# Kernel optimization log

Measured on AMD Instinct MI355X. Metric: run time of the kernel, lower is better.

## Reference

```python
import jax, jax.numpy as jnp
import numpy as np

D_EMB, N_HEADS = 1024, 16
D_K = D_EMB // N_HEADS

def setup_inputs() -> dict:
    key = jax.random.key(0)
    ks = jax.random.split(key, 5)
    scale = 0.02
    return {
        "n": jax.random.normal(ks[0], (2, 2048, D_EMB), dtype=jnp.float32),
        "W_q": jax.random.normal(ks[1], (D_EMB, D_EMB), dtype=jnp.float32) * scale,
        "W_k": jax.random.normal(ks[2], (D_EMB, D_EMB), dtype=jnp.float32) * scale,
        "W_v": jax.random.normal(ks[3], (D_EMB, D_EMB), dtype=jnp.float32) * scale,
        "W_o": jax.random.normal(ks[4], (D_EMB, D_EMB), dtype=jnp.float32) * scale,
    }

def reference(n, W_q, W_k, W_v, W_o):
    B, S, _ = n.shape
    # torch Linear(bias=False): y = x @ W.T, W is [out, in]
    def proj(x, W):
        y = jnp.einsum('bsd,ed->bse', x, W)
        return y.reshape(B, S, N_HEADS, D_K).transpose(0, 2, 1, 3)  # [B,H,S,Dk]
    Q, K, V = proj(n, W_q), proj(n, W_k), proj(n, W_v)
    A = jnp.einsum('bhqd,bhkd->bhqk', Q, K) * (D_K ** -0.5)
    A = jnp.clip(A, -5.0, 5.0)
    A = jax.nn.softmax(A, axis=-1)
    ctx = jnp.einsum('bhqk,bhkd->bhqd', A, V)  # [B,H,S,Dk]
    ctx = ctx.transpose(0, 2, 1, 3).reshape(B, S, D_EMB)
    return jnp.einsum('bsd,ed->bse', ctx, W_o)
```

## Files before the change

kernel.cpp:

```cpp
#include <hip/hip_runtime.h>
#include <hip/hip_bf16.h>
#include <stdint.h>

typedef __attribute__((ext_vector_type(4))) float floatx4;
typedef __attribute__((ext_vector_type(8))) short shortx8;
typedef __attribute__((ext_vector_type(4))) unsigned short ushortx4;
typedef __attribute__((ext_vector_type(8))) unsigned short ushortx8;
typedef __attribute__((ext_vector_type(2))) uint32_t uintx2;

#define MFMA16(a, b, c) __builtin_amdgcn_mfma_f32_16x16x32_bf16((a), (b), (c), 0, 0, 0)

__device__ inline unsigned short f2bf(float f) {
    union { float f; uint32_t u; } v; v.f = f;
    uint32_t u = v.u;
    return (unsigned short)((u + 0x7FFFu + ((u >> 16) & 1u)) >> 16);
}

#if defined(__has_builtin) && __has_builtin(__builtin_amdgcn_cvt_pk_bf16_f32)
__device__ inline uint32_t pkbf(float a, float b) {
    auto r = __builtin_amdgcn_cvt_pk_bf16_f32(a, b);
    union { decltype(r) v; uint32_t u; } x; x.v = r; return x.u;
}
#else
__device__ inline uint32_t pkbf(float a, float b) {
    return ((uint32_t)f2bf(b) << 16) | f2bf(a);
}
#endif

#if defined(__has_builtin) && __has_builtin(__builtin_amdgcn_exp2f)
#define EXP2F(x) __builtin_amdgcn_exp2f(x)
#else
#define EXP2F(x) __expf((x) * 0.69314718056f)
#endif

#if defined(__has_builtin) && __has_builtin(__builtin_amdgcn_fmed3f)
#define CLAMP3(x, lo, hi) __builtin_amdgcn_fmed3f((x), (lo), (hi))
#else
#define CLAMP3(x, lo, hi) fminf(fmaxf((x), (lo)), (hi))
#endif

__device__ inline void gl2lds16(const void* g, void* l) {
    __builtin_amdgcn_global_load_lds(
        (const __attribute__((address_space(1))) void*)(uintptr_t)g,
        (__attribute__((address_space(3))) void*)(uintptr_t)l, 16, 0, 0);
}

__global__ void convert_all(const float* __restrict__ n, const float* __restrict__ wq,
                            const float* __restrict__ wk, const float* __restrict__ wv,
                            const float* __restrict__ wo,
                            unsigned short* __restrict__ nb, unsigned short* __restrict__ wqb,
                            unsigned short* __restrict__ wkb, unsigned short* __restrict__ wvb,
                            unsigned short* __restrict__ wob) {
    int i = blockIdx.x * 256 + threadIdx.x;
    const float* src; unsigned short* dst; int off;
    if (i < 1048576) { src = n; dst = nb; off = i; }
    else {
        int j = i - 1048576; int r = j >> 18; int o = j & 262143;
        src = (r == 0) ? wq : (r == 1) ? wk : (r == 2) ? wv : wo;
        dst = (r == 0) ? wqb : (r == 1) ? wkb : (r == 2) ? wvb : wob;
        off = o;
    }
    floatx4 f = ((const floatx4*)src)[off];
    uintx2 u;
    u.x = pkbf(f.x, f.y); u.y = pkbf(f.z, f.w);
    ((uintx2*)dst)[off] = u;
}

__device__ inline void gemm_tile_128(const unsigned short* __restrict__ A,
                                     const unsigned short* __restrict__ B,
                                     unsigned short* sA, unsigned short* sB,
                                     floatx4 acc[4][4]) {
    const int tid = threadIdx.x, w = tid >> 6, l = tid & 63;
    const int c = l & 15, quad = l >> 4;
    const int wm = (w >> 1) * 64, wn = (w & 1) * 64;
    for (int kt = 0; kt < 16; ++kt) {
        #pragma unroll
        for (int r = 0; r < 4; ++r) {
            int row = r * 32 + w * 8 + (l >> 3);
            int cb  = (l & 7) ^ (row & 7);
            gl2lds16(A + row * 1024 + kt * 64 + cb * 8, (char*)sA + r * 4096 + w * 1024 + l * 16);
            gl2lds16(B + row * 1024 + kt * 64 + cb * 8, (char*)sB + r * 4096 + w * 1024 + l * 16);
        }
        __syncthreads();
        #pragma unroll
        for (int ks = 0; ks < 2; ++ks) {
            shortx8 af[4], bfr[4];
            #pragma unroll
            for (int i2 = 0; i2 < 4; ++i2) {
                int ra = wm + i2 * 16 + c;
                af[i2] = *(const shortx8*)((const char*)sA + ra * 128 + (((ks * 4 + quad) ^ (ra & 7)) * 16));
                int rb = wn + i2 * 16 + c;
                bfr[i2] = *(const shortx8*)((const char*)sB + rb * 128 + (((ks * 4 + quad) ^ (rb & 7)) * 16));
            }
            #pragma unroll
            for (int i2 = 0; i2 < 4; ++i2)
                #pragma unroll
                for (int j2 = 0; j2 < 4; ++j2)
                    acc[i2][j2] = MFMA16(af[i2], bfr[j2], acc[i2][j2]);
        }
        __syncthreads();
    }
}

__global__ void gemm_qkv(const unsigned short* __restrict__ nb,
                         const unsigned short* __restrict__ wqb,
                         const unsigned short* __restrict__ wkb,
                         const unsigned short* __restrict__ wvb,
                         unsigned short* __restrict__ Qb, unsigned short* __restrict__ Kb,
                         unsigned short* __restrict__ VTg) {
    __shared__ unsigned short sAB[2 * 128 * 64];
    unsigned short* sA = sAB;
    unsigned short* sB = sAB + 128 * 64;
    const int mt = blockIdx.x, nt = blockIdx.y;
    const int region = nt >> 3, nl0 = (nt & 7) * 128;
    const unsigned short* W = (region == 0) ? wqb : (region == 1) ? wkb : wvb;
    floatx4 acc[4][4] = {};
    gemm_tile_128(nb + mt * 128 * 1024, W + nl0 * 1024, sA, sB, acc);
    const int tid = threadIdx.x, w = tid >> 6, l = tid & 63, c = l & 15, quad = l >> 4;
    const int wm = (w >> 1) * 64, wn = (w & 1) * 64;
    if (region < 2) {
        unsigned short* O = (region == 0) ? Qb : Kb;
        #pragma unroll
        for (int i2 = 0; i2 < 4; ++i2)
            #pragma unroll
            for (int j2 = 0; j2 < 4; ++j2)
                #pragma unroll
                for (int r = 0; r < 4; ++r) {
                    int row = wm + i2 * 16 + quad * 4 + r, col = wn + j2 * 16 + c;
                    sAB[row * 128 + col] = f2bf(acc[i2][j2][r]);
                }
        __syncthreads();
        #pragma unroll
        for (int t = 0; t < 8; ++t) {
            int off = t * 4096 + tid * 16;
            int row = off >> 8, colb = off & 255;
            *(ushortx8*)((char*)(O + (mt * 128 + row) * 1024 + nl0) + colb) =
                *(const ushortx8*)((const char*)sAB + off);
        }
    } else {
        const int hh = w & 1, tt = w >> 1;
        char* img = (char*)sAB + (hh * 2 + tt) * 8192;
        #pragma unroll
        for (int i2 = 0; i2 < 4; ++i2)
            #pragma unroll
            for (int j2 = 0; j2 < 4; ++j2) {
                int d = j2 * 16 + c;
                int blk = (i2 >> 1) * 4 + quad;
                int phys = blk ^ (d & 7);
                uintx2 v;
                v.x = pkbf(acc[i2][j2][0], acc[i2][j2][1]);
                v.y = pkbf(acc[i2][j2][2], acc[i2][j2][3]);
                *(uintx2*)(img + d * 128 + phys * 16 + (i2 & 1) * 8) = v;
            }
        __syncthreads();
        const int h0 = (nt & 7) * 2, t0 = mt * 2;
        #pragma unroll
        for (int g = 0; g < 8; ++g) {
            int off = g * 4096 + tid * 16;
            int hsel = off >> 14, within = off & 16383;
            *(ushortx8*)((char*)VTg + (h0 + hsel) * 524288 + t0 * 8192 + within) =
                *(const ushortx8*)((const char*)sAB + off);
        }
    }
}

__global__ void __launch_bounds__(256) gemm_out(const unsigned short* __restrict__ ctx,
                         const unsigned short* __restrict__ wob,
                         float* __restrict__ out) {
    __shared__ unsigned short sA[128 * 64];
    __shared__ unsigned short sB[64 * 64];
    __shared__ float sC[64 * 64];
    const int mt = blockIdx.x, nt = blockIdx.y;
    const unsigned short* A = ctx + mt * 128 * 1024;
    const unsigned short* B = wob + nt * 64 * 1024;
    const int tid = threadIdx.x, w = tid >> 6, l = tid & 63, c = l & 15, quad = l >> 4;
    const int srow = w * 8 + (l >> 3), scb = l & 7;
    floatx4 acc[2][4] = {};
    for (int kt = 0; kt < 16; ++kt) {
        #pragma unroll
        for (int r = 0; r < 4; ++r) {
            int row = r * 32 + srow, cb = scb ^ (row & 7);
            gl2lds16(A + row * 1024 + kt * 64 + cb * 8, (char*)sA + r * 4096 + w * 1024 + l * 16);
        }
        #pragma unroll
        for (int r = 0; r < 2; ++r) {
            int row = r * 32 + srow, cb = scb ^ (row & 7);
            gl2lds16(B + row * 1024 + kt * 64 + cb * 8, (char*)sB + r * 4096 + w * 1024 + l * 16);
        }
        __syncthreads();
        #pragma unroll
        for (int ks = 0; ks < 2; ++ks) {
            shortx8 af[2], bf2[4];
            #pragma unroll
            for (int i2 = 0; i2 < 2; ++i2) {
                int ra = w * 32 + i2 * 16 + c;
                af[i2] = *(const shortx8*)((const char*)sA + ra * 128 + (((ks * 4 + quad) ^ (ra & 7)) * 16));
            }
            #pragma unroll
            for (int j2 = 0; j2 < 4; ++j2) {
                int rb = j2 * 16 + c;
                bf2[j2] = *(const shortx8*)((const char*)sB + rb * 128 + (((ks * 4 + quad) ^ (rb & 7)) * 16));
            }
            #pragma unroll
            for (int i2 = 0; i2 < 2; ++i2)
                #pragma unroll
                for (int j2 = 0; j2 < 4; ++j2)
                    acc[i2][j2] = MFMA16(af[i2], bf2[j2], acc[i2][j2]);
        }
        __syncthreads();
    }
    #pragma unroll
    for (int half = 0; half < 2; ++half) {
        if ((w >> 1) == half) {
            #pragma unroll
            for (int i2 = 0; i2 < 2; ++i2)
                #pragma unroll
                for (int j2 = 0; j2 < 4; ++j2)
                    #pragma unroll
                    for (int r = 0; r < 4; ++r) {
                        int row = (w & 1) * 32 + i2 * 16 + quad * 4 + r, col = j2 * 16 + c;
                        sC[row * 64 + col] = acc[i2][j2][r];
                    }
        }
        __syncthreads();
        #pragma unroll
        for (int t = 0; t < 4; ++t) {
            int off = t * 4096 + tid * 16;
            int row = off >> 8, colb = off & 255;
            *(floatx4*)((char*)(out + (mt * 128 + half * 64 + row) * 1024 + nt * 64) + colb) =
                *(const floatx4*)((const char*)sC + off);
        }
        __syncthreads();
    }
}

__global__ void __launch_bounds__(256, 2) attn(const unsigned short* __restrict__ Qb,
                     const unsigned short* __restrict__ Kb,
                     const unsigned short* __restrict__ VTg, unsigned short* __restrict__ ctx) {
    __shared__ char lds[81920];
    const int qt = blockIdx.x, h = blockIdx.y, b = blockIdx.z;
    const int tid = threadIdx.x, w = tid >> 6, l = tid & 63, c = l & 15, quad = l >> 4;
    const int tok0 = b * 2048 + qt * 128;
    const int srow = w * 8 + (l >> 3);
    const int cb = (l & 7) ^ (srow & 7);
    #pragma unroll
    for (int r = 0; r < 4; ++r)
        gl2lds16(Qb + (tok0 + r * 32 + srow) * 1024 + h * 64 + cb * 8, lds + r * 4096 + w * 1024 + l * 16);
    const unsigned short* Kbase = Kb + b * 2048 * 1024 + h * 64;
    const char* Vbase = (const char*)VTg + h * 524288 + (size_t)b * 262144;
    const char* Ksrc = (const char*)(Kbase + srow * 1024 + cb * 8);
    #define STAGE_K(kt, t) { _Pragma("unroll") for (int r = 0; r < 2; ++r) \
        gl2lds16(Ksrc + (size_t)(kt) * 131072 + r * 65536, lds + 16384 + (t) * 8192 + r * 4096 + w * 1024 + l * 16); }
    #define STAGE_V(kt, t) { _Pragma("unroll") for (int r = 0; r < 2; ++r) \
        gl2lds16(Vbase + (kt) * 8192 + r * 4096 + w * 1024 + l * 16, lds + 49152 + (t) * 8192 + r * 4096 + w * 1024 + l * 16); }
    STAGE_K(0, 0) STAGE_V(0, 0) STAGE_K(1, 1) STAGE_V(1, 1)
    __syncthreads();
    int lb[2];
    lb[0] = c * 128 + ((quad ^ (c & 7)) * 16);
    lb[1] = c * 128 + (((4 + quad) ^ (c & 7)) * 16);
    shortx8 qf[2][2];
    #pragma unroll
    for (int ks = 0; ks < 2; ++ks)
        #pragma unroll
        for (int qb = 0; qb < 2; ++qb)
            qf[ks][qb] = *(const shortx8*)(lds + (w * 2 + qb) * 2048 + lb[ks]);
    floatx4 cacc[4][2] = {};
    float lacc[2] = {0.f, 0.f};
    const float SC = 0.18033688f;
    const float CLIP = 7.2134752f;

    #define COMPUTE_S(t, s) { _Pragma("unroll") for (int ks = 0; ks < 2; ++ks) { \
        shortx8 ak[4]; \
        _Pragma("unroll") for (int j = 0; j < 4; ++j) \
            ak[j] = *(const shortx8*)(lds + 16384 + (t) * 8192 + j * 2048 + lb[ks]); \
        _Pragma("unroll") for (int j = 0; j < 4; ++j) \
            _Pragma("unroll") for (int qb = 0; qb < 2; ++qb) \
                s[qb][j] = MFMA16(ak[j], qf[ks][qb], s[qb][j]); } }

    #define SOFTMAX_T(s) { _Pragma("unroll") for (int qb = 0; qb < 2; ++qb) { \
        float rs = 0.f; \
        _Pragma("unroll") for (int j = 0; j < 4; ++j) \
            _Pragma("unroll") for (int r = 0; r < 4; ++r) { \
                float v = EXP2F(CLAMP3(s[qb][j][r] * SC, -CLIP, CLIP)); \
                s[qb][j][r] = v; rs += v; } \
        rs += __shfl_xor(rs, 16); rs += __shfl_xor(rs, 32); \
        lacc[qb] += rs; } }

    #define PV_T(t, s) { _Pragma("unroll") for (int chunk = 0; chunk < 2; ++chunk) { \
        shortx8 av[4]; \
        _Pragma("unroll") for (int di = 0; di < 4; ++di) \
            av[di] = *(const shortx8*)(lds + 49152 + (t) * 8192 + di * 2048 + lb[chunk]); \
        shortx8 p[2]; \
        _Pragma("unroll") for (int qb = 0; qb < 2; ++qb) { \
            union { shortx8 v; uint32_t u[4]; } pk; \
            pk.u[0] = pkbf(s[qb][2 * chunk][0], s[qb][2 * chunk][1]); \
            pk.u[1] = pkbf(s[qb][2 * chunk][2], s[qb][2 * chunk][3]); \
            pk.u[2] = pkbf(s[qb][2 * chunk + 1][0], s[qb][2 * chunk + 1][1]); \
            pk.u[3] = pkbf(s[qb][2 * chunk + 1][2], s[qb][2 * chunk + 1][3]); \
            p[qb] = pk.v; } \
        _Pragma("unroll") for (int di = 0; di < 4; ++di) \
            _Pragma("unroll") for (int qb = 0; qb < 2; ++qb) \
                cacc[di][qb] = MFMA16(av[di], p[qb], cacc[di][qb]); } }

    for (int p = 0; p < 16; ++p) {
        const int bufA = (p & 1) * 2, bufB = bufA + 1;
        if (p < 15) {
            const int nA = bufA ^ 2;
            STAGE_K(2 * p + 2, nA) STAGE_V(2 * p + 2, nA)
            STAGE_K(2 * p + 3, nA + 1) STAGE_V(2 * p + 3, nA + 1)
        }
        floatx4 sA[2][4] = {}, sB[2][4] = {};
        COMPUTE_S(bufA, sA)
        COMPUTE_S(bufB, sB)
        SOFTMAX_T(sA)
        PV_T(bufA, sA)
        SOFTMAX_T(sB)
        PV_T(bufB, sB)
        if (p < 15) __syncthreads();
    }
    #pragma unroll
    for (int qb = 0; qb < 2; ++qb) {
        float inv = 1.0f / lacc[qb];
        int row = tok0 + w * 32 + qb * 16 + c;
        #pragma unroll
        for (int di = 0; di < 4; ++di) {
            uintx2 v;
            v.x = pkbf(cacc[di][qb][0] * inv, cacc[di][qb][1] * inv);
            v.y = pkbf(cacc[di][qb][2] * inv, cacc[di][qb][3] * inv);
            *(uintx2*)(ctx + row * 1024 + h * 64 + di * 16 + quad * 4) = v;
        }
    }
}

extern "C" void kernel_launch(void* const* d_in, const int* in_sizes, int n_in,
                              void* d_out, int out_size, void* d_ws, size_t ws_size,
                              hipStream_t stream) {
    const float* n  = (const float*)d_in[0];
    const float* wq = (const float*)d_in[1];
    const float* wk = (const float*)d_in[2];
    const float* wv = (const float*)d_in[3];
    const float* wo = (const float*)d_in[4];
    float* out = (float*)d_out;
    char* ws = (char*)d_ws;
    unsigned short* nb  = (unsigned short*)(ws);
    unsigned short* wqb = (unsigned short*)(ws + 8388608);
    unsigned short* wkb = (unsigned short*)(ws + 10485760);
    unsigned short* wvb = (unsigned short*)(ws + 12582912);
    unsigned short* wob = (unsigned short*)(ws + 14680064);
    unsigned short* Qb  = (unsigned short*)(ws + 16777216);
    unsigned short* Kb  = (unsigned short*)(ws + 25165824);
    unsigned short* VTg = (unsigned short*)(ws + 33554432);
    unsigned short* ctx = (unsigned short*)(ws + 41943040);

    convert_all<<<dim3(8192), dim3(256), 0, stream>>>(n, wq, wk, wv, wo, nb, wqb, wkb, wvb, wob);
    gemm_qkv<<<dim3(32, 24), dim3(256), 0, stream>>>(nb, wqb, wkb, wvb, Qb, Kb, VTg);
    attn<<<dim3(16, 16, 2), dim3(256), 0, stream>>>(Qb, Kb, VTg, ctx);
    gemm_out<<<dim3(32, 16), dim3(256), 0, stream>>>(ctx, wob, out);
}
```

Baseline: 177.0 us.

## Load K fragments directly from global memory and fold softmax scale into Q

The attention kernel stops staging K tiles through LDS. Each lane now reads its K MFMA fragments straight from global memory, which cuts LDS from 80KB to 48KB and drops the K copy traffic. The softmax scale is folded into Q at the QKV GEMM epilogue, which removes a multiply per score element. The cost is uncoalesced 16-byte global loads of K whose latency sits directly in front of the score MFMAs with no prefetch. Rounding Q to bf16 after scaling may also change numerics slightly.

```diff
diff --git a/kernel.cpp b/kernel.cpp
--- a/kernel.cpp
+++ b/kernel.cpp
@@ -120,6 +120,7 @@
     const int wm = (w >> 1) * 64, wn = (w & 1) * 64;
     if (region < 2) {
         unsigned short* O = (region == 0) ? Qb : Kb;
+        const float sc = (region == 0) ? 0.18033688f : 1.0f;
         #pragma unroll
         for (int i2 = 0; i2 < 4; ++i2)
             #pragma unroll
@@ -127,7 +128,7 @@
                 #pragma unroll
                 for (int r = 0; r < 4; ++r) {
                     int row = wm + i2 * 16 + quad * 4 + r, col = wn + j2 * 16 + c;
-                    sAB[row * 128 + col] = f2bf(acc[i2][j2][r]);
+                    sAB[row * 128 + col] = f2bf(acc[i2][j2][r] * sc);
                 }
         __syncthreads();
         #pragma unroll
@@ -237,7 +238,7 @@
 __global__ void __launch_bounds__(256, 2) attn(const unsigned short* __restrict__ Qb,
                      const unsigned short* __restrict__ Kb,
                      const unsigned short* __restrict__ VTg, unsigned short* __restrict__ ctx) {
-    __shared__ char lds[81920];
+    __shared__ char lds[49152];
     const int qt = blockIdx.x, h = blockIdx.y, b = blockIdx.z;
     const int tid = threadIdx.x, w = tid >> 6, l = tid & 63, c = l & 15, quad = l >> 4;
     const int tok0 = b * 2048 + qt * 128;
@@ -246,14 +247,11 @@
     #pragma unroll
     for (int r = 0; r < 4; ++r)
         gl2lds16(Qb + (tok0 + r * 32 + srow) * 1024 + h * 64 + cb * 8, lds + r * 4096 + w * 1024 + l * 16);
-    const unsigned short* Kbase = Kb + b * 2048 * 1024 + h * 64;
     const char* Vbase = (const char*)VTg + h * 524288 + (size_t)b * 262144;
-    const char* Ksrc = (const char*)(Kbase + srow * 1024 + cb * 8);
-    #define STAGE_K(kt, t) { _Pragma("unroll") for (int r = 0; r < 2; ++r) \
-        gl2lds16(Ksrc + (size_t)(kt) * 131072 + r * 65536, lds + 16384 + (t) * 8192 + r * 4096 + w * 1024 + l * 16); }
+    const char* Klane = (const char*)(Kb + (size_t)b * 2048 * 1024 + h * 64) + c * 2048 + quad * 16;
     #define STAGE_V(kt, t) { _Pragma("unroll") for (int r = 0; r < 2; ++r) \
-        gl2lds16(Vbase + (kt) * 8192 + r * 4096 + w * 1024 + l * 16, lds + 49152 + (t) * 8192 + r * 4096 + w * 1024 + l * 16); }
-    STAGE_K(0, 0) STAGE_V(0, 0) STAGE_K(1, 1) STAGE_V(1, 1)
+        gl2lds16(Vbase + (kt) * 8192 + r * 4096 + w * 1024 + l * 16, lds + 16384 + (t) * 8192 + r * 4096 + w * 1024 + l * 16); }
+    STAGE_V(0, 0) STAGE_V(1, 1)
     __syncthreads();
     int lb[2];
     lb[0] = c * 128 + ((quad ^ (c & 7)) * 16);
@@ -266,22 +264,28 @@
             qf[ks][qb] = *(const shortx8*)(lds + (w * 2 + qb) * 2048 + lb[ks]);
     floatx4 cacc[4][2] = {};
     float lacc[2] = {0.f, 0.f};
-    const float SC = 0.18033688f;
     const float CLIP = 7.2134752f;
-
-    #define COMPUTE_S(t, s) { _Pragma("unroll") for (int ks = 0; ks < 2; ++ks) { \
+    const floatx4 fz = {0.f, 0.f, 0.f, 0.f};
+
+    #define COMPUTE_S_G(kt, s) { \
+        const char* Kt = Klane + (size_t)(kt) * 131072; \
         shortx8 ak[4]; \
         _Pragma("unroll") for (int j = 0; j < 4; ++j) \
-            ak[j] = *(const shortx8*)(lds + 16384 + (t) * 8192 + j * 2048 + lb[ks]); \
+            ak[j] = *(const shortx8*)(Kt + j * 32768); \
         _Pragma("unroll") for (int j = 0; j < 4; ++j) \
             _Pragma("unroll") for (int qb = 0; qb < 2; ++qb) \
-                s[qb][j] = MFMA16(ak[j], qf[ks][qb], s[qb][j]); } }
+                s[qb][j] = MFMA16(ak[j], qf[0][qb], fz); \
+        _Pragma("unroll") for (int j = 0; j < 4; ++j) \
+            ak[j] = *(const shortx8*)(Kt + j * 32768 + 64); \
+        _Pragma("unroll") for (int j = 0; j < 4; ++j) \
+            _Pragma("unroll") for (int qb = 0; qb < 2; ++qb) \
+                s[qb][j] = MFMA16(ak[j], qf[1][qb], s[qb][j]); }
 
     #define SOFTMAX_T(s) { _Pragma("unroll") for (int qb = 0; qb < 2; ++qb) { \
         float rs = 0.f; \
         _Pragma("unroll") for (int j = 0; j < 4; ++j) \
             _Pragma("unroll") for (int r = 0; r < 4; ++r) { \
-                float v = EXP2F(CLAMP3(s[qb][j][r] * SC, -CLIP, CLIP)); \
+                float v = EXP2F(CLAMP3(s[qb][j][r], -CLIP, CLIP)); \
                 s[qb][j][r] = v; rs += v; } \
         rs += __shfl_xor(rs, 16); rs += __shfl_xor(rs, 32); \
         lacc[qb] += rs; } }
@@ -289,7 +293,7 @@
     #define PV_T(t, s) { _Pragma("unroll") for (int chunk = 0; chunk < 2; ++chunk) { \
         shortx8 av[4]; \
         _Pragma("unroll") for (int di = 0; di < 4; ++di) \
-            av[di] = *(const shortx8*)(lds + 49152 + (t) * 8192 + di * 2048 + lb[chunk]); \
+            av[di] = *(const shortx8*)(lds + 16384 + (t) * 8192 + di * 2048 + lb[chunk]); \
         shortx8 p[2]; \
         _Pragma("unroll") for (int qb = 0; qb < 2; ++qb) { \
             union { shortx8 v; uint32_t u[4]; } pk; \
@@ -306,12 +310,11 @@
         const int bufA = (p & 1) * 2, bufB = bufA + 1;
         if (p < 15) {
             const int nA = bufA ^ 2;
-            STAGE_K(2 * p + 2, nA) STAGE_V(2 * p + 2, nA)
-            STAGE_K(2 * p + 3, nA + 1) STAGE_V(2 * p + 3, nA + 1)
-        }
-        floatx4 sA[2][4] = {}, sB[2][4] = {};
-        COMPUTE_S(bufA, sA)
-        COMPUTE_S(bufB, sB)
+            STAGE_V(2 * p + 2, nA) STAGE_V(2 * p + 3, nA + 1)
+        }
+        floatx4 sA[2][4], sB[2][4];
+        COMPUTE_S_G(2 * p, sA)
+        COMPUTE_S_G(2 * p + 1, sB)
         SOFTMAX_T(sA)
         PV_T(bufA, sA)
         SOFTMAX_T(sB)
```

Measured after the change: 203.7 us. 15.1% more time.
